# Performance work log

Hardware: AMD Instinct MI355X
Metric: run time of the kernel (lower is better)

The kernel has to match this reference:

```python
import jax, jax.numpy as jnp
import numpy as np

GRID_SIZE = 16
KH = KW = 3


def setup_inputs() -> dict:
    key = jax.random.key(0)
    k1, k2, k3, k4 = jax.random.split(key, 4)
    B, H, W, C, F = 8, 32, 32, 64, 64
    x = jax.random.normal(k1, (B, H, W, C), dtype=jnp.float32)
    control_points = jax.random.normal(k2, (F, C, KH, KW, GRID_SIZE), dtype=jnp.float32) * 0.1
    w1 = jax.random.normal(k3, (F, C, KH, KW), dtype=jnp.float32) * 0.1
    w2 = jax.random.normal(k4, (F, C, KH, KW), dtype=jnp.float32) * 0.1
    return {"x": x, "control_points": control_points, "w1": w1, "w2": w2}


def _extract_patches_same(x, kh, kw):
    # x: (B,H,W,C), stride 1, TF 'SAME' padding -> (B,H,W,kh,kw,C)
    B, H, W, C = x.shape
    ph, pw = kh - 1, kw - 1
    xp = jnp.pad(x, ((0, 0), (ph // 2, ph - ph // 2), (pw // 2, pw - pw // 2), (0, 0)))
    taps = [xp[:, i:i + H, j:j + W, :] for i in range(kh) for j in range(kw)]
    return jnp.stack(taps, axis=3).reshape(B, H, W, kh, kw, C)


def reference(x, control_points, w1, w2):
    F, C, kh, kw, G = control_points.shape
    grid = jnp.linspace(-1.0, 1.0, G)
    patches = _extract_patches_same(x, kh, kw)  # (B,H,W,kh,kw,C)
    # spline: searchsorted + clip + linear interp on the fixed uniform grid
    xc = jnp.clip(patches, -1.0, 1.0)
    idx = jnp.clip(jnp.searchsorted(grid, xc, side='left') - 1, 0, G - 2)
    frac = (xc - grid[idx]) / (grid[idx + 1] - grid[idx])  # (B,H,W,kh,kw,C)
    # two-nonzero linear basis over control points -> (B,H,W,kh,kw,C,G)
    basis = (jax.nn.one_hot(idx, G, dtype=x.dtype) * (1.0 - frac)[..., None]
             + jax.nn.one_hot(idx + 1, G, dtype=x.dtype) * frac[..., None])
    # fuse w1 into control points, contract taps+channels+grid in one einsum
    wcp = w1[..., None] * control_points  # (F,C,kh,kw,G)
    out = jnp.einsum('bpqijcg,fcijg->bpqf', basis, wcp)
    out = out + jnp.einsum('bpqijc,fcij->bpqf', jax.nn.silu(patches), w2)
    return out  # (B,H,W,F)
```

## Files before the change

### kernel.cpp

```cpp
#include <hip/hip_runtime.h>


typedef _Float16 v8h __attribute__((ext_vector_type(8)));
typedef float    v4f __attribute__((ext_vector_type(4)));

#define NSLOT8  81920
#define NOUT4   131072

__global__ __launch_bounds__(256) void prep_wsw(const float* __restrict__ cp,
                                                const float* __restrict__ w1,
                                                const float* __restrict__ w2,
                                                _Float16* __restrict__ wsw,
                                                float* __restrict__ out) {
    int tid = blockIdx.x * 256 + threadIdx.x;
    if (tid < NSLOT8) {
        int lane = tid & 63;
        int rest = tid >> 6;
        int nt   = rest & 3;
        int ks   = rest >> 2;
        int kb   = ks * 32 + ((lane >> 4) << 3);
        int f    = (nt << 4) + (lane & 15);
        int chunk = kb / 640;
        int klb   = kb - chunk * 640;
        v8h o;
        if (klb < 576) {
            int c  = (chunk << 2) + klb / 144;
            int rb = klb % 144;
            int ij = rb >> 4;
            float w = w1[f * 576 + c * 9 + ij];
            const v4f* cpp = (const v4f*)(cp + (size_t)f * 9216 + c * 144 + rb);
            v4f lo = cpp[0], hi = cpp[1];
#pragma unroll
            for (int j = 0; j < 4; ++j) {
                o[j]     = (_Float16)(w * lo[j]);
                o[j + 4] = (_Float16)(w * hi[j]);
            }
        } else {
            int i2 = klb - 576;
            int c  = (chunk << 2) + (i2 >> 4);
            if ((i2 & 15) == 0) {
#pragma unroll
                for (int j = 0; j < 8; ++j)
                    o[j] = (_Float16)w2[f * 576 + c * 9 + j];
            } else {
#pragma unroll
                for (int j = 0; j < 8; ++j) o[j] = (_Float16)0.f;
                o[0] = (_Float16)w2[f * 576 + c * 9 + 8];
            }
        }
        ((v8h*)wsw)[tid] = o;
    }
    if (tid < NOUT4) ((v4f*)out)[tid] = (v4f){0.f, 0.f, 0.f, 0.f};
}

__global__ __launch_bounds__(256, 4) void kan_mfma(const float* __restrict__ x,
                                                   const _Float16* __restrict__ wsw,
                                                   float* __restrict__ out) {
    __shared__ __align__(16) char smem[40960];
    float* red = (float*)smem;

    int blk   = blockIdx.x;
    int kh    = blk >> 8;
    int rowid = blk & 255;
    int b = rowid >> 5, p = rowid & 31;
    int t = threadIdx.x, wv = t >> 6, lane = t & 63;
    int m = lane & 15, kq = lane >> 4;

    int ch0 = kh * 4, ch1 = ch0 + 4;
    const float* xb = x + (size_t)b * 65536;

    int xoff[2], sbase[2], smask[2], ijb[2];
    bool act[2];
#pragma unroll
    for (int it = 0; it < 2; ++it) {
        bool a = (it == 0) || (lane < 8);
        int e  = a ? (wv * 72 + it * 64 + lane) : 0;
        int q  = e / 9;
        int ij = e - q * 9;
        int di = ij / 3;
        int dj = ij - di * 3;
        int row = p + di - 1;
        int col = q + dj - 1;
        bool ok = ((unsigned)row < 32u) && ((unsigned)col < 32u) && a;
        act[it]   = a;
        xoff[it]  = ok ? (row * 32 + col) * 64 : -1;
        sbase[it] = q * 1280;
        smask[it] = (q & 7) << 4;
        ijb[it]   = ij * 32;
    }

    v4f z4 = (v4f){0.f, 0.f, 0.f, 0.f};
    v4f acc[2][4];
#pragma unroll
    for (int i = 0; i < 2; ++i)
#pragma unroll
        for (int n = 0; n < 4; ++n) acc[i][n] = z4;

    for (int i4 = t; i4 < 2560; i4 += 256) ((v4f*)smem)[i4] = z4;

    v4f vbuf[2];
#pragma unroll
    for (int it = 0; it < 2; ++it)
        vbuf[it] = (xoff[it] >= 0) ? *(const v4f*)(xb + xoff[it] + ch0 * 4) : z4;
    unsigned pk[2] = {0u, 0u};

    __syncthreads();

    for (int gch = ch0; gch < ch1; ++gch) {
#pragma unroll
        for (int it = 0; it < 2; ++it) {
            if (act[it]) {
                v4f xv = vbuf[it];
                char* rowp = smem + sbase[it];
                int mask = smask[it];
                int jb   = ijb[it];
                unsigned pp = pk[it], np = 0;
#pragma unroll
                for (int cl = 0; cl < 4; ++cl) {
                    float v  = xv[cl];
                    float xc = fminf(fmaxf(v, -1.f), 1.f);
                    float tt = (xc + 1.f) * 7.5f;
                    int idx  = (int)tt;
                    if (idx > 14) idx = 14;
                    float fr = tt - (float)idx;
                    float sv = v * __builtin_amdgcn_rcpf(1.f + __expf(-v));
                    int sb0 = cl * 288 + jb;
                    if (gch > ch0) {
                        int pb = sb0 + (int)((pp >> (cl * 8)) & 255) * 2;
                        *(_Float16*)(rowp + (pb ^ mask))       = (_Float16)0.f;
                        *(_Float16*)(rowp + ((pb + 2) ^ mask)) = (_Float16)0.f;
                    }
                    int wb = sb0 + idx * 2;
                    *(_Float16*)(rowp + (wb ^ mask))       = (_Float16)(1.f - fr);
                    *(_Float16*)(rowp + ((wb + 2) ^ mask)) = (_Float16)fr;
                    *(_Float16*)(rowp + ((1152 + cl * 32 + (jb >> 4)) ^ mask))
                        = (_Float16)sv;
                    np |= (unsigned)idx << (cl * 8);
                }
                pk[it] = np;
            }
        }
        __syncthreads();
        if (gch + 1 < ch1) {
#pragma unroll
            for (int it = 0; it < 2; ++it)
                vbuf[it] = (xoff[it] >= 0)
                         ? *(const v4f*)(xb + xoff[it] + (gch + 1) * 4) : z4;
        }
        const v8h* bp = (const v8h*)wsw + ((size_t)gch * 20 + wv * 5) * 256 + lane;
        int mbase = m * 1280;
        int mm    = (m & 7) << 4;
#pragma unroll
        for (int s = 0; s < 5; ++s) {
            int kx = (((wv * 5 + s) * 64) + (kq * 16)) ^ mm;
            v8h a0 = *(const v8h*)(smem + mbase + kx);
            v8h a1 = *(const v8h*)(smem + mbase + 20480 + kx);
            v8h b0 = bp[s * 256];
            v8h b1 = bp[s * 256 + 64];
            v8h b2 = bp[s * 256 + 128];
            v8h b3 = bp[s * 256 + 192];
            acc[0][0] = __builtin_amdgcn_mfma_f32_16x16x32_f16(a0, b0, acc[0][0], 0, 0, 0);
            acc[0][1] = __builtin_amdgcn_mfma_f32_16x16x32_f16(a0, b1, acc[0][1], 0, 0, 0);
            acc[0][2] = __builtin_amdgcn_mfma_f32_16x16x32_f16(a0, b2, acc[0][2], 0, 0, 0);
            acc[0][3] = __builtin_amdgcn_mfma_f32_16x16x32_f16(a0, b3, acc[0][3], 0, 0, 0);
            acc[1][0] = __builtin_amdgcn_mfma_f32_16x16x32_f16(a1, b0, acc[1][0], 0, 0, 0);
            acc[1][1] = __builtin_amdgcn_mfma_f32_16x16x32_f16(a1, b1, acc[1][1], 0, 0, 0);
            acc[1][2] = __builtin_amdgcn_mfma_f32_16x16x32_f16(a1, b2, acc[1][2], 0, 0, 0);
            acc[1][3] = __builtin_amdgcn_mfma_f32_16x16x32_f16(a1, b3, acc[1][3], 0, 0, 0);
        }
        __syncthreads();
    }

#pragma unroll
    for (int mt = 0; mt < 2; ++mt)
#pragma unroll
        for (int nt = 0; nt < 4; ++nt)
#pragma unroll
            for (int r = 0; r < 4; ++r)
                red[wv * 2080 + (mt * 16 + kq * 4 + r) * 65 + nt * 16 + m] = acc[mt][nt][r];
    __syncthreads();
    int f = t & 63, pxg = t >> 6;
    float* op = out + (size_t)rowid * 2048 + f;
#pragma unroll
    for (int i = 0; i < 8; ++i) {
        int px = pxg * 8 + i;
        float s = red[px * 65 + f] + red[2080 + px * 65 + f]
                + red[4160 + px * 65 + f] + red[6240 + px * 65 + f];
        atomicAdd(op + px * 64, s);
    }
}

extern "C" void kernel_launch(void* const* d_in, const int* in_sizes, int n_in,
                              void* d_out, int out_size, void* d_ws, size_t ws_size,
                              hipStream_t stream) {
    const float* x  = (const float*)d_in[0];
    const float* cp = (const float*)d_in[1];
    const float* w1 = (const float*)d_in[2];
    const float* w2 = (const float*)d_in[3];
    _Float16* wsw = (_Float16*)d_ws;
    float*    outp = (float*)d_out;

    prep_wsw<<<512, 256, 0, stream>>>(cp, w1, w2, wsw, outp);
    kan_mfma<<<1024, 256, 0, stream>>>(x, wsw, outp);
}
```

Before: 83.00 us.

## Double block to 512 threads, splitting N tiles across wave pairs

The MFMA kernel now runs 512 threads per block. Each pair of waves shares a K-slice, and each wave computes half the output-feature tiles (2 of 4), so per-wave accumulators and B loads are halved. The patch-building stage also maps one element per thread (288 active), replacing two iterations per thread. The aim is more waves in flight per CU to hide latency, at the cost of A fragments being read twice from LDS and larger block-wide barriers.

```diff
diff --git a/kernel.cpp b/kernel.cpp
--- a/kernel.cpp
+++ b/kernel.cpp
@@ -53,7 +53,7 @@
     if (tid < NOUT4) ((v4f*)out)[tid] = (v4f){0.f, 0.f, 0.f, 0.f};
 }
 
-__global__ __launch_bounds__(256, 4) void kan_mfma(const float* __restrict__ x,
+__global__ __launch_bounds__(512, 8) void kan_mfma(const float* __restrict__ x,
                                                    const _Float16* __restrict__ wsw,
                                                    float* __restrict__ out) {
     __shared__ __align__(16) char smem[40960];
@@ -65,108 +65,89 @@
     int b = rowid >> 5, p = rowid & 31;
     int t = threadIdx.x, wv = t >> 6, lane = t & 63;
     int m = lane & 15, kq = lane >> 4;
+    int wg = wv >> 1, nh = wv & 1;
 
     int ch0 = kh * 4, ch1 = ch0 + 4;
     const float* xb = x + (size_t)b * 65536;
 
-    int xoff[2], sbase[2], smask[2], ijb[2];
-    bool act[2];
-#pragma unroll
-    for (int it = 0; it < 2; ++it) {
-        bool a = (it == 0) || (lane < 8);
-        int e  = a ? (wv * 72 + it * 64 + lane) : 0;
+    bool act = t < 288;
+    int xoff, sbase, smask, ijb;
+    {
+        int e  = act ? t : 0;
         int q  = e / 9;
         int ij = e - q * 9;
         int di = ij / 3;
         int dj = ij - di * 3;
         int row = p + di - 1;
         int col = q + dj - 1;
-        bool ok = ((unsigned)row < 32u) && ((unsigned)col < 32u) && a;
-        act[it]   = a;
-        xoff[it]  = ok ? (row * 32 + col) * 64 : -1;
-        sbase[it] = q * 1280;
-        smask[it] = (q & 7) << 4;
-        ijb[it]   = ij * 32;
+        bool ok = ((unsigned)row < 32u) && ((unsigned)col < 32u) && act;
+        xoff  = ok ? (row * 32 + col) * 64 : -1;
+        sbase = q * 1280;
+        smask = (q & 7) << 4;
+        ijb   = ij * 32;
     }
 
     v4f z4 = (v4f){0.f, 0.f, 0.f, 0.f};
-    v4f acc[2][4];
+    v4f acc[2][2];
 #pragma unroll
     for (int i = 0; i < 2; ++i)
 #pragma unroll
-        for (int n = 0; n < 4; ++n) acc[i][n] = z4;
+        for (int n = 0; n < 2; ++n) acc[i][n] = z4;
 
-    for (int i4 = t; i4 < 2560; i4 += 256) ((v4f*)smem)[i4] = z4;
+    for (int i4 = t; i4 < 2560; i4 += 512) ((v4f*)smem)[i4] = z4;
 
-    v4f vbuf[2];
-#pragma unroll
-    for (int it = 0; it < 2; ++it)
-        vbuf[it] = (xoff[it] >= 0) ? *(const v4f*)(xb + xoff[it] + ch0 * 4) : z4;
-    unsigned pk[2] = {0u, 0u};
+    v4f vbuf = (xoff >= 0) ? *(const v4f*)(xb + xoff + ch0 * 4) : z4;
+    unsigned pk = 0u;
 
     __syncthreads();
 
     for (int gch = ch0; gch < ch1; ++gch) {
+        if (act) {
+            v4f xv = vbuf;
+            char* rowp = smem + sbase;
+            unsigned pp = pk, np = 0;
 #pragma unroll
-        for (int it = 0; it < 2; ++it) {
-            if (act[it]) {
-                v4f xv = vbuf[it];
-                char* rowp = smem + sbase[it];
-                int mask = smask[it];
-                int jb   = ijb[it];
-                unsigned pp = pk[it], np = 0;
-#pragma unroll
-                for (int cl = 0; cl < 4; ++cl) {
-                    float v  = xv[cl];
-                    float xc = fminf(fmaxf(v, -1.f), 1.f);
-                    float tt = (xc + 1.f) * 7.5f;
-                    int idx  = (int)tt;
-                    if (idx > 14) idx = 14;
-                    float fr = tt - (float)idx;
-                    float sv = v * __builtin_amdgcn_rcpf(1.f + __expf(-v));
-                    int sb0 = cl * 288 + jb;
-                    if (gch > ch0) {
-                        int pb = sb0 + (int)((pp >> (cl * 8)) & 255) * 2;
-                        *(_Float16*)(rowp + (pb ^ mask))       = (_Float16)0.f;
-                        *(_Float16*)(rowp + ((pb + 2) ^ mask)) = (_Float16)0.f;
-                    }
-                    int wb = sb0 + idx * 2;
-                    *(_Float16*)(rowp + (wb ^ mask))       = (_Float16)(1.f - fr);
-                    *(_Float16*)(rowp + ((wb + 2) ^ mask)) = (_Float16)fr;
-                    *(_Float16*)(rowp + ((1152 + cl * 32 + (jb >> 4)) ^ mask))
-                        = (_Float16)sv;
-                    np |= (unsigned)idx << (cl * 8);
+            for (int cl = 0; cl < 4; ++cl) {
+                float v  = xv[cl];
+                float xc = fminf(fmaxf(v, -1.f), 1.f);
+                float tt = (xc + 1.f) * 7.5f;
+                int idx  = (int)tt;
+                if (idx > 14) idx = 14;
+                float fr = tt - (float)idx;
+                float sv = v * __builtin_amdgcn_rcpf(1.f + __expf(-v));
+                int sb0 = cl * 288 + ijb;
+                if (gch > ch0) {
+                    int pb = sb0 + (int)((pp >> (cl * 8)) & 255) * 2;
+                    *(_Float16*)(rowp + (pb ^ smask))       = (_Float16)0.f;
+                    *(_Float16*)(rowp + ((pb + 2) ^ smask)) = (_Float16)0.f;
                 }
-                pk[it] = np;
+                int wb = sb0 + idx * 2;
+                *(_Float16*)(rowp + (wb ^ smask))       = (_Float16)(1.f - fr);
+                *(_Float16*)(rowp + ((wb + 2) ^ smask)) = (_Float16)fr;
+                *(_Float16*)(rowp + ((1152 + cl * 32 + (ijb >> 4)) ^ smask))
+                    = (_Float16)sv;
+                np |= (unsigned)idx << (cl * 8);
             }
+            pk = np;
         }
         __syncthreads();
-        if (gch + 1 < ch1) {
-#pragma unroll
-            for (int it = 0; it < 2; ++it)
-                vbuf[it] = (xoff[it] >= 0)
-                         ? *(const v4f*)(xb + xoff[it] + (gch + 1) * 4) : z4;
-        }
-        const v8h* bp = (const v8h*)wsw + ((size_t)gch * 20 + wv * 5) * 256 + lane;
+        if (gch + 1 < ch1)
+            vbuf = (xoff >= 0) ? *(const v4f*)(xb + xoff + (gch + 1) * 4) : z4;
+        const v8h* bp = (const v8h*)wsw
+                      + ((size_t)gch * 20 + wg * 5) * 256 + nh * 128 + lane;
         int mbase = m * 1280;
         int mm    = (m & 7) << 4;
 #pragma unroll
         for (int s = 0; s < 5; ++s) {
-            int kx = (((wv * 5 + s) * 64) + (kq * 16)) ^ mm;
+            int kx = (((wg * 5 + s) * 64) + (kq * 16)) ^ mm;
             v8h a0 = *(const v8h*)(smem + mbase + kx);
             v8h a1 = *(const v8h*)(smem + mbase + 20480 + kx);
             v8h b0 = bp[s * 256];
             v8h b1 = bp[s * 256 + 64];
-            v8h b2 = bp[s * 256 + 128];
-            v8h b3 = bp[s * 256 + 192];
             acc[0][0] = __builtin_amdgcn_mfma_f32_16x16x32_f16(a0, b0, acc[0][0], 0, 0, 0);
             acc[0][1] = __builtin_amdgcn_mfma_f32_16x16x32_f16(a0, b1, acc[0][1], 0, 0, 0);
-            acc[0][2] = __builtin_amdgcn_mfma_f32_16x16x32_f16(a0, b2, acc[0][2], 0, 0, 0);
-            acc[0][3] = __builtin_amdgcn_mfma_f32_16x16x32_f16(a0, b3, acc[0][3], 0, 0, 0);
             acc[1][0] = __builtin_amdgcn_mfma_f32_16x16x32_f16(a1, b0, acc[1][0], 0, 0, 0);
             acc[1][1] = __builtin_amdgcn_mfma_f32_16x16x32_f16(a1, b1, acc[1][1], 0, 0, 0);
-            acc[1][2] = __builtin_amdgcn_mfma_f32_16x16x32_f16(a1, b2, acc[1][2], 0, 0, 0);
-            acc[1][3] = __builtin_amdgcn_mfma_f32_16x16x32_f16(a1, b3, acc[1][3], 0, 0, 0);
         }
         __syncthreads();
     }
@@ -174,16 +155,17 @@
 #pragma unroll
     for (int mt = 0; mt < 2; ++mt)
 #pragma unroll
-        for (int nt = 0; nt < 4; ++nt)
+        for (int ntl = 0; ntl < 2; ++ntl)
 #pragma unroll
             for (int r = 0; r < 4; ++r)
-                red[wv * 2080 + (mt * 16 + kq * 4 + r) * 65 + nt * 16 + m] = acc[mt][nt][r];
+                red[wg * 2080 + (mt * 16 + kq * 4 + r) * 65
+                    + (nh * 2 + ntl) * 16 + m] = acc[mt][ntl][r];
     __syncthreads();
-    int f = t & 63, pxg = t >> 6;
+    int f = t & 63, pg = t >> 6;
     float* op = out + (size_t)rowid * 2048 + f;
 #pragma unroll
-    for (int i = 0; i < 8; ++i) {
-        int px = pxg * 8 + i;
+    for (int i = 0; i < 4; ++i) {
+        int px = pg * 4 + i;
         float s = red[px * 65 + f] + red[2080 + px * 65 + f]
                 + red[4160 + px * 65 + f] + red[6240 + px * 65 + f];
         atomicAdd(op + px * 64, s);
@@ -201,5 +183,5 @@
     float*    outp = (float*)d_out;
 
     prep_wsw<<<512, 256, 0, stream>>>(cp, w1, w2, wsw, outp);
-    kan_mfma<<<1024, 256, 0, stream>>>(x, wsw, outp);
+    kan_mfma<<<1024, 512, 0, stream>>>(x, wsw, outp);
 }
```

Result: no change. 82.18 us, median of 2 (-1.0%).
